# Kernel optimization log

Hardware: AMD Instinct MI355X
Metric: run time of the kernel (lower is better)

## Reference

```python
import jax, jax.numpy as jnp
import numpy as np

B, S, H, E = 2, 4096, 2048, 8


def setup_inputs() -> dict:
    key = jax.random.key(0)
    k1, k2, k3 = jax.random.split(key, 3)
    x = jax.random.normal(k1, (B, S, H), dtype=jnp.float32)
    w_router = jax.random.normal(k2, (E, H), dtype=jnp.float32) * (1.0 / np.sqrt(H))
    # nn.Linear weight layout: [out_features, in_features] per expert -> [E, H, H]
    w_experts = jax.random.normal(k3, (E, H, H), dtype=jnp.float32) * (1.0 / np.sqrt(H))
    return {"x": x, "w_router": w_router, "w_experts": w_experts}


def reference(x, w_router, w_experts):
    # router logits: x @ W_r^T  -> [B, S, E]
    logits = jnp.einsum('bsh,eh->bse', x, w_router)
    idx = jnp.argmax(logits, axis=-1)  # [B, S] top-1 expert per token
    # dense all-expert outputs (matches original which evaluates every expert):
    # expert_e(x) = x @ W_e^T -> [B, S, E, H]
    all_out = jnp.einsum('bsh,efh->bsef', x, w_experts)
    # masked sum over one-hot mask == gather of the selected expert output
    out = jnp.take_along_axis(all_out, idx[:, :, None, None], axis=2)[:, :, 0, :]
    return out
```

## Files before the change

### kernel.cpp

```cpp
#include <hip/hip_runtime.h>
#include <hip/hip_bf16.h>
#include <cstdint>

#define T_TOK 8192
#define H_DIM 2048
#define N_EXP 8
#define FLAGBIT 0x80000000u

typedef __attribute__((ext_vector_type(4))) float f32x4;
typedef __attribute__((ext_vector_type(8))) short bf16x8;

__device__ __forceinline__ unsigned short f2bf(float f) {
  unsigned int u = __builtin_bit_cast(unsigned int, f);
  u += 0x7fffu + ((u >> 16) & 1u);
  return (unsigned short)(u >> 16);
}

__device__ __forceinline__ unsigned cvtpk(float lo, float hi) {
  unsigned r;
  asm("v_cvt_pk_bf16_f32 %0, %1, %2" : "=v"(r) : "v"(lo), "v"(hi));
  return r;
}

#define GLL(SRC, DST) __builtin_amdgcn_global_load_lds( \
    (const __attribute__((address_space(1))) void*)(SRC), \
    (__attribute__((address_space(3))) void*)(DST), 16, 0, 0)

__global__ __launch_bounds__(256) void k_pre(const float* __restrict__ x,
    const float* __restrict__ wr, const float* __restrict__ we,
    unsigned short* __restrict__ xb, unsigned short* __restrict__ wb,
    int* __restrict__ idx)
{
  __shared__ char smem[65536];
  const int bid = blockIdx.x;
  if (bid >= 512) {
    auto* LDS3 = (__attribute__((address_space(3))) char*)smem;
    const char* LP = (const char*)smem;
    const int wv = threadIdx.x >> 6, l = threadIdx.x & 63;
    const size_t base = (size_t)(bid - 512) * 131072;
    const char* src = (const char*)we + base + wv * 8192 + l * 16;
    unsigned short* dstp = wb + (base >> 2) + wv * 2048 + l * 4;
#pragma unroll
    for (int i = 0; i < 8; ++i)
      GLL(src + i * 1024, LDS3 + wv * 8192 + i * 1024);
    for (int c = 0; c < 4; ++c) {
      const int b = (c & 1) * 32768;
      if (c < 3) {
        const char* s2 = src + (c + 1) * 32768;
        auto* d2 = LDS3 + (b ^ 32768) + wv * 8192;
#pragma unroll
        for (int i = 0; i < 8; ++i) GLL(s2 + i * 1024, d2 + i * 1024);
        asm volatile("s_waitcnt vmcnt(8)" ::: "memory");
      } else {
        asm volatile("s_waitcnt vmcnt(0)" ::: "memory");
      }
#pragma unroll
      for (int i = 0; i < 8; ++i) {
        const f32x4 v = *reinterpret_cast<const f32x4*>(LP + b + wv * 8192 + i * 1024 + l * 16);
        uint2 r;
        r.x = cvtpk(v[0], v[1]);
        r.y = cvtpk(v[2], v[3]);
        *reinterpret_cast<uint2*>(dstp + c * 8192 + i * 256) = r;
      }
    }
    return;
  }
  float* swr = (float*)smem;
#pragma unroll
  for (int i = 0; i < 16; ++i) {
    const int o = (threadIdx.x + i * 256) * 4;
    *reinterpret_cast<float4*>(&swr[o]) = *reinterpret_cast<const float4*>(&wr[o]);
  }
  __syncthreads();
  const int wv = threadIdx.x >> 6, lane = threadIdx.x & 63;
  const int t0 = (bid * 4 + wv) * 4;
  float acc[4][N_EXP];
#pragma unroll
  for (int tt = 0; tt < 4; ++tt)
#pragma unroll
    for (int e = 0; e < N_EXP; ++e) acc[tt][e] = 0.f;
#pragma unroll
  for (int c = 0; c < H_DIM / 256; ++c) {
    const int h = c * 256 + lane * 4;
    float4 wvv[N_EXP];
#pragma unroll
    for (int e = 0; e < N_EXP; ++e)
      wvv[e] = *reinterpret_cast<const float4*>(&swr[e * H_DIM + h]);
#pragma unroll
    for (int tt = 0; tt < 4; ++tt) {
      const float4 xv = *reinterpret_cast<const float4*>(x + (size_t)(t0 + tt) * H_DIM + h);
      ushort4 bv;
      bv.x = f2bf(xv.x); bv.y = f2bf(xv.y); bv.z = f2bf(xv.z); bv.w = f2bf(xv.w);
      *reinterpret_cast<ushort4*>(xb + (size_t)(t0 + tt) * H_DIM + h) = bv;
#pragma unroll
      for (int e = 0; e < N_EXP; ++e) {
        acc[tt][e] = fmaf(xv.x, wvv[e].x, acc[tt][e]);
        acc[tt][e] = fmaf(xv.y, wvv[e].y, acc[tt][e]);
        acc[tt][e] = fmaf(xv.z, wvv[e].z, acc[tt][e]);
        acc[tt][e] = fmaf(xv.w, wvv[e].w, acc[tt][e]);
      }
    }
  }
#pragma unroll
  for (int off = 32; off >= 1; off >>= 1)
#pragma unroll
    for (int tt = 0; tt < 4; ++tt)
#pragma unroll
      for (int e = 0; e < N_EXP; ++e) acc[tt][e] += __shfl_xor(acc[tt][e], off, 64);
  if (lane == 0) {
#pragma unroll
    for (int tt = 0; tt < 4; ++tt) {
      float best = acc[tt][0]; int be = 0;
#pragma unroll
      for (int e = 1; e < N_EXP; ++e) if (acc[tt][e] > best) { best = acc[tt][e]; be = e; }
      idx[t0 + tt] = be;
    }
  }
}

__global__ __launch_bounds__(1024) void k_sort(const int* __restrict__ idx,
    int* __restrict__ tlist, int* __restrict__ estar, int* __restrict__ mlo,
    int* __restrict__ mhi, int* __restrict__ rpos, int* __restrict__ rtile,
    int* __restrict__ rtc)
{
  __shared__ int wc[N_EXP][128];
  __shared__ int wbase[N_EXP][128];
  __shared__ int sTot[N_EXP];
  __shared__ int off[N_EXP + 1];
  __shared__ int sE[32], sCnt[N_EXP], sBase[N_EXP];
  const int tid = threadIdx.x, w = tid >> 6, l = tid & 63;
  int myE[8];
#pragma unroll
  for (int j = 0; j < 8; ++j) {
    myE[j] = idx[j * 1024 + tid];
#pragma unroll
    for (int e = 0; e < N_EXP; ++e) {
      const unsigned long long bm = __ballot(myE[j] == e);
      if (l == e) wc[e][j * 16 + w] = __popcll(bm);
    }
  }
  __syncthreads();
  if (tid < N_EXP) {
    int s = 0;
    for (int k = 0; k < 128; ++k) { wbase[tid][k] = s; s += wc[tid][k]; }
    sTot[tid] = s;
  }
  __syncthreads();
  if (tid == 0) {
    off[0] = 0;
    for (int e = 0; e < N_EXP; ++e) off[e + 1] = off[e] + sTot[e];
  }
  __syncthreads();
#pragma unroll
  for (int j = 0; j < 8; ++j) {
    int rank = 0;
#pragma unroll
    for (int e = 0; e < N_EXP; ++e) {
      const unsigned long long bm = __ballot(myE[j] == e);
      if (myE[j] == e) rank = __popcll(bm & ((1ull << l) - 1ull));
    }
    tlist[off[myE[j]] + wbase[myE[j]][j * 16 + w] + rank] = j * 1024 + tid;
  }
  if (tid < 32) {
    const int lo = tid * 256, hi = lo + 256;
    int bl = -1, bE = 0, bLo = 0, bHi = 0;
#pragma unroll
    for (int e = 0; e < N_EXP; ++e) {
      const int a = off[e] > lo ? off[e] : lo;
      const int b = off[e + 1] < hi ? off[e + 1] : hi;
      if (b - a > bl) { bl = b - a; bE = e; bLo = a - lo; bHi = b - lo; }
    }
    sE[tid] = bE; estar[tid] = bE; mlo[tid] = bLo; mhi[tid] = bHi;
  }
  __syncthreads();
  if (tid < N_EXP) {
    int cnt = 0;
    for (int t = 0; t < 32; ++t) {
      if (sE[t] == tid) continue;
      const int lo = t * 256, hi = lo + 256;
      const int a = off[tid] > lo ? off[tid] : lo;
      const int b = off[tid + 1] < hi ? off[tid + 1] : hi;
      if (b > a) cnt += b - a;
    }
    sCnt[tid] = cnt;
  }
  __syncthreads();
  if (tid == 0) {
    int base = 0, ntile = 0;
    for (int e = 0; e < N_EXP; ++e) {
      sBase[e] = base;
      const int pt = (sCnt[e] + 127) >> 7;
      for (int k = 0; k < pt; ++k) rtile[ntile++] = e;
      base += pt << 7;
    }
    *rtc = ntile;
  }
  __syncthreads();
  if (tid < N_EXP && sCnt[tid] > 0) {
    int ptr = sBase[tid], firstp = -1;
    for (int t = 0; t < 32; ++t) {
      if (sE[t] == tid) continue;
      const int lo = t * 256, hi = lo + 256;
      const int a = off[tid] > lo ? off[tid] : lo;
      const int b = off[tid + 1] < hi ? off[tid + 1] : hi;
      for (int p = a; p < b; ++p) { if (firstp < 0) firstp = p; rpos[ptr++] = p; }
    }
    const int end = sBase[tid] + (((sCnt[tid] + 127) >> 7) << 7);
    for (; ptr < end; ++ptr) rpos[ptr] = (int)((unsigned)firstp | FLAGBIT);
  }
}

__global__ __launch_bounds__(256) void k_zero_min(const int* __restrict__ rpos,
    const int* __restrict__ tlist, const int* __restrict__ rtc,
    float* __restrict__ out)
{
  const int nslots = (*rtc) << 7;
  const float4 z = {0.f, 0.f, 0.f, 0.f};
  for (int s = blockIdx.x; s < nslots; s += 256) {
    const int ent = rpos[s];
    if ((unsigned)ent & FLAGBIT) continue;
    const int tok = tlist[ent];
    float* op = out + (size_t)tok * H_DIM;
    for (int i = threadIdx.x; i < H_DIM / 4; i += 256)
      reinterpret_cast<float4*>(op)[i] = z;
  }
}

__global__ __launch_bounds__(1024, 4) void k_gemm(const unsigned short* __restrict__ xb,
    const unsigned short* __restrict__ wb, const int* __restrict__ tlist,
    const int* __restrict__ estar, const int* __restrict__ mlo, const int* __restrict__ mhi,
    const int* __restrict__ rpos, const int* __restrict__ rtile, const int* __restrict__ rtc,
    float* __restrict__ out)
{
  __shared__ short lds[65536];
  const int bid = blockIdx.x;
  const int tid = threadIdx.x;
  const int l = tid & 63, wv = tid >> 6;
  const int l16 = l & 15, g16 = l >> 4;
  const char* LP = (const char*)lds;
  auto* LDS3 = (__attribute__((address_space(3))) char*)lds;

  if (bid < 256) {
    const int mt = (bid & 7) * 4 + ((bid >> 3) & 3);
    const int nt = bid >> 5;
    const int m0 = mt * 256, f0 = nt * 256;
    const int e = estar[mt], mLo = mlo[mt], mHi = mhi[mt];
    const int wm = wv >> 2, wn = wv & 3;

    const int ch = (g16 ^ ((l16 >> 1) & 3)) << 4;
    const int aRd = (wm * 64 + l16) * 64 + ch;
    const int bRd = 16384 + (wn * 64 + l16) * 64 + ch;

    const int csrc = (((l & 3) ^ ((l >> 3) & 3))) * 8;
    const int srow = l >> 2;
    const int tokA = tlist[m0 + wv * 16 + srow];
    const unsigned short* aS = xb + (size_t)tokA * H_DIM + csrc;
    const unsigned short* bS = wb + (size_t)e * H_DIM * H_DIM
                                  + (size_t)(f0 + wv * 16 + srow) * H_DIM + csrc;
    const int dA = wv * 1024;
    const int dB = 16384 + wv * 1024;

    f32x4 acc[4][4];
#pragma unroll
    for (int mf = 0; mf < 4; ++mf)
#pragma unroll
      for (int nf = 0; nf < 4; ++nf) acc[mf][nf] = (f32x4){0.f, 0.f, 0.f, 0.f};

    GLL(aS +  0, LDS3 + 0 * 32768 + dA);  GLL(bS +  0, LDS3 + 0 * 32768 + dB);
    GLL(aS + 32, LDS3 + 1 * 32768 + dA);  GLL(bS + 32, LDS3 + 1 * 32768 + dB);
    GLL(aS + 64, LDS3 + 2 * 32768 + dA);  GLL(bS + 64, LDS3 + 2 * 32768 + dB);
    asm volatile("s_waitcnt vmcnt(4)" ::: "memory");
    __builtin_amdgcn_sched_barrier(0);
    __builtin_amdgcn_s_barrier();
    __builtin_amdgcn_sched_barrier(0);

    for (int t = 0; t < 64; ++t) {
      const int buf  = (t & 3) * 32768;
      const int nbuf = ((t + 3) & 3) * 32768;
      const int kk   = ((t + 3) & 63) * 32;
      bf16x8 af[4], bf[4];
#pragma unroll
      for (int mf = 0; mf < 4; ++mf)
        af[mf] = *reinterpret_cast<const bf16x8*>(LP + buf + aRd + mf * 1024);
#pragma unroll
      for (int nf = 0; nf < 4; ++nf)
        bf[nf] = *reinterpret_cast<const bf16x8*>(LP + buf + bRd + nf * 1024);
      GLL(aS + kk, LDS3 + nbuf + dA);
      GLL(bS + kk, LDS3 + nbuf + dB);
      __builtin_amdgcn_s_setprio(1);
#pragma unroll
      for (int mf = 0; mf < 4; ++mf)
#pragma unroll
        for (int nf = 0; nf < 4; ++nf)
          acc[mf][nf] = __builtin_amdgcn_mfma_f32_16x16x32_bf16(af[mf], bf[nf], acc[mf][nf], 0, 0, 0);
      __builtin_amdgcn_s_setprio(0);
      asm volatile("s_waitcnt vmcnt(4)" ::: "memory");
      __builtin_amdgcn_sched_barrier(0);
      __builtin_amdgcn_s_barrier();
      __builtin_amdgcn_sched_barrier(0);
    }

#pragma unroll
    for (int mf = 0; mf < 4; ++mf) {
#pragma unroll
      for (int r = 0; r < 4; ++r) {
        const int row = wm * 64 + mf * 16 + g16 * 4 + r;
        if (row >= mLo && row < mHi) {
          const int t2 = tlist[m0 + row];
          float* op = out + (size_t)t2 * H_DIM + f0 + wn * 64 + l16;
#pragma unroll
          for (int nf = 0; nf < 4; ++nf) op[nf * 16] = acc[mf][nf][r];
        }
      }
    }
    return;
  }

  const int bid2 = bid - 256;
  const int bx = bid2 >> 4;
  if (bx >= *rtc) return;
  const int f0 = ((bid2 >> 1) & 7) * 256;
  const int kc = bid2 & 1;
  const int e = rtile[bx];
  const int wm = wv >> 2, wn = wv & 3;
  const int sw = l16 & 7;
  const int ch0 = ((0 + g16) ^ sw) << 4, ch1 = ((4 + g16) ^ sw) << 4;
  const int csrc8 = ((l & 7) ^ ((l >> 3) & 7)) * 8;
  const int srow8 = l >> 3;

  const unsigned short* aS;
  {
    const int ent = rpos[bx * 128 + wv * 8 + srow8];
    const int tok = tlist[ent & 0x7fffffff];
    aS = xb + (size_t)tok * H_DIM + csrc8;
  }
  const unsigned short* bS0 = wb + (size_t)e * H_DIM * H_DIM
                                 + (size_t)(f0 + wv * 8 + srow8) * H_DIM + csrc8;
  const unsigned short* bS1 = bS0 + (size_t)128 * H_DIM;

  f32x4 acc[2][4];
#pragma unroll
  for (int mf = 0; mf < 2; ++mf)
#pragma unroll
    for (int nf = 0; nf < 4; ++nf) acc[mf][nf] = (f32x4){0.f, 0.f, 0.f, 0.f};

  for (int it = 0; it < 16; ++it) {
    const int kk = kc * 1024 + it * 64;
    __syncthreads();
    GLL(aS + kk, LDS3 + wv * 1024);
    GLL(bS0 + kk, LDS3 + 16384 + wv * 1024);
    GLL(bS1 + kk, LDS3 + 16384 + 16384 + wv * 1024);
    __syncthreads();
    bf16x8 af[2][2];
#pragma unroll
    for (int mf = 0; mf < 2; ++mf) {
      af[mf][0] = *reinterpret_cast<const bf16x8*>(LP + (wm * 32 + mf * 16 + l16) * 128 + ch0);
      af[mf][1] = *reinterpret_cast<const bf16x8*>(LP + (wm * 32 + mf * 16 + l16) * 128 + ch1);
    }
#pragma unroll
    for (int nf = 0; nf < 4; ++nf) {
      const bf16x8 b0 = *reinterpret_cast<const bf16x8*>(LP + 16384 + (wn * 64 + nf * 16 + l16) * 128 + ch0);
      const bf16x8 b1 = *reinterpret_cast<const bf16x8*>(LP + 16384 + (wn * 64 + nf * 16 + l16) * 128 + ch1);
#pragma unroll
      for (int mf = 0; mf < 2; ++mf) {
        acc[mf][nf] = __builtin_amdgcn_mfma_f32_16x16x32_bf16(af[mf][0], b0, acc[mf][nf], 0, 0, 0);
        acc[mf][nf] = __builtin_amdgcn_mfma_f32_16x16x32_bf16(af[mf][1], b1, acc[mf][nf], 0, 0, 0);
      }
    }
  }
#pragma unroll
  for (int mf = 0; mf < 2; ++mf) {
#pragma unroll
    for (int r = 0; r < 4; ++r) {
      const int row = wm * 32 + mf * 16 + g16 * 4 + r;
      const int ent = rpos[bx * 128 + row];
      if (!((unsigned)ent & FLAGBIT)) {
        const int tok = tlist[ent];
        float* op = out + (size_t)tok * H_DIM + f0 + wn * 64 + l16;
#pragma unroll
        for (int nf = 0; nf < 4; ++nf) atomicAdd(op + nf * 16, acc[mf][nf][r]);
      }
    }
  }
}

extern "C" void kernel_launch(void* const* d_in, const int* in_sizes, int n_in,
                              void* d_out, int out_size, void* d_ws, size_t ws_size,
                              hipStream_t stream) {
  const float* x  = (const float*)d_in[0];
  const float* wr = (const float*)d_in[1];
  const float* we = (const float*)d_in[2];
  float* out = (float*)d_out;

  char* p = (char*)d_ws;
  unsigned short* xb = (unsigned short*)p; p += (size_t)T_TOK * H_DIM * 2;
  unsigned short* wb = (unsigned short*)p; p += (size_t)N_EXP * H_DIM * H_DIM * 2;
  int* idx    = (int*)p; p += T_TOK * 4;
  int* tlist  = (int*)p; p += T_TOK * 4;
  int* rpos   = (int*)p; p += T_TOK * 4;
  int* estar  = (int*)p; p += 32 * 4;
  int* mlo    = (int*)p; p += 32 * 4;
  int* mhi    = (int*)p; p += 32 * 4;
  int* rtile  = (int*)p; p += 64 * 4;
  int* rtc    = (int*)p; p += 64;

  k_pre<<<512 + 1024, 256, 0, stream>>>(x, wr, we, xb, wb, idx);
  k_sort<<<1, 1024, 0, stream>>>(idx, tlist, estar, mlo, mhi, rpos, rtile, rtc);
  k_zero_min<<<256, 256, 0, stream>>>(rpos, tlist, rtc, out);
  k_gemm<<<256 + 1024, 1024, 0, stream>>>(xb, wb, tlist, estar, mlo, mhi, rpos, rtile, rtc, out);
}
```

Baseline: 184.1 us.

## Shrink GEMM workgroups to 256 threads with 128x128 tiles and more blocks

The main grouped GEMM now uses 256-thread workgroups computing 128x128 output tiles instead of 1024-thread workgroups on 256x256 tiles. Each wave issues twice as many async global-to-LDS loads, and LDS use is halved. The remainder path for mixed-expert tiles is reworked the same way: 4 waves, K step 32 instead of 64, and a 4x8 fragment accumulator per wave. The aim is more concurrent blocks per CU and better latency hiding, at the cost of less data reuse per tile and more blocks to schedule.

```diff
diff --git a/kernel.cpp b/kernel.cpp
--- a/kernel.cpp
+++ b/kernel.cpp
@@ -226,39 +226,49 @@
   }
 }
 
-__global__ __launch_bounds__(1024, 4) void k_gemm(const unsigned short* __restrict__ xb,
+__global__ __launch_bounds__(256) void k_gemm(const unsigned short* __restrict__ xb,
     const unsigned short* __restrict__ wb, const int* __restrict__ tlist,
     const int* __restrict__ estar, const int* __restrict__ mlo, const int* __restrict__ mhi,
     const int* __restrict__ rpos, const int* __restrict__ rtile, const int* __restrict__ rtc,
     float* __restrict__ out)
 {
-  __shared__ short lds[65536];
+  __shared__ short lds[32768];
   const int bid = blockIdx.x;
   const int tid = threadIdx.x;
   const int l = tid & 63, wv = tid >> 6;
   const int l16 = l & 15, g16 = l >> 4;
   const char* LP = (const char*)lds;
   auto* LDS3 = (__attribute__((address_space(3))) char*)lds;
-
-  if (bid < 256) {
-    const int mt = (bid & 7) * 4 + ((bid >> 3) & 3);
-    const int nt = bid >> 5;
-    const int m0 = mt * 256, f0 = nt * 256;
-    const int e = estar[mt], mLo = mlo[mt], mHi = mhi[mt];
-    const int wm = wv >> 2, wn = wv & 3;
-
-    const int ch = (g16 ^ ((l16 >> 1) & 3)) << 4;
+  const int csrc = ((l & 3) ^ ((l >> 3) & 3)) * 8;
+  const int ch = (g16 ^ ((l16 >> 1) & 3)) << 4;
+
+  if (bid < 1024) {
+    const int idx8 = bid >> 3;
+    const int mt = (bid & 7) * 8 + (idx8 >> 4);
+    const int nt = idx8 & 15;
+    const int m0 = mt * 128, f0 = nt * 128;
+    const int par = mt >> 1, half = (mt & 1) * 128;
+    const int e = estar[par];
+    const int mLo = mlo[par] - half, mHi = mhi[par] - half;
+    const int wm = wv >> 1, wn = wv & 1;
+
     const int aRd = (wm * 64 + l16) * 64 + ch;
-    const int bRd = 16384 + (wn * 64 + l16) * 64 + ch;
-
-    const int csrc = (((l & 3) ^ ((l >> 3) & 3))) * 8;
+    const int bRd = 8192 + (wn * 64 + l16) * 64 + ch;
+
     const int srow = l >> 2;
-    const int tokA = tlist[m0 + wv * 16 + srow];
-    const unsigned short* aS = xb + (size_t)tokA * H_DIM + csrc;
-    const unsigned short* bS = wb + (size_t)e * H_DIM * H_DIM
-                                  + (size_t)(f0 + wv * 16 + srow) * H_DIM + csrc;
-    const int dA = wv * 1024;
-    const int dB = 16384 + wv * 1024;
+    const unsigned short* aS[2];
+#pragma unroll
+    for (int j = 0; j < 2; ++j) {
+      const int tok = tlist[m0 + wv * 32 + j * 16 + srow];
+      aS[j] = xb + (size_t)tok * H_DIM + csrc;
+    }
+    const unsigned short* bS[2];
+#pragma unroll
+    for (int j = 0; j < 2; ++j)
+      bS[j] = wb + (size_t)e * H_DIM * H_DIM
+                 + (size_t)(f0 + wv * 32 + j * 16 + srow) * H_DIM + csrc;
+    const int dA0 = wv * 2048, dA1 = wv * 2048 + 1024;
+    const int dB0 = 8192 + wv * 2048, dB1 = 8192 + wv * 2048 + 1024;
 
     f32x4 acc[4][4];
 #pragma unroll
@@ -266,17 +276,20 @@
 #pragma unroll
       for (int nf = 0; nf < 4; ++nf) acc[mf][nf] = (f32x4){0.f, 0.f, 0.f, 0.f};
 
-    GLL(aS +  0, LDS3 + 0 * 32768 + dA);  GLL(bS +  0, LDS3 + 0 * 32768 + dB);
-    GLL(aS + 32, LDS3 + 1 * 32768 + dA);  GLL(bS + 32, LDS3 + 1 * 32768 + dB);
-    GLL(aS + 64, LDS3 + 2 * 32768 + dA);  GLL(bS + 64, LDS3 + 2 * 32768 + dB);
-    asm volatile("s_waitcnt vmcnt(4)" ::: "memory");
+#pragma unroll
+    for (int t0i = 0; t0i < 3; ++t0i) {
+      const int bb = t0i * 16384, kk = t0i * 32;
+      GLL(aS[0] + kk, LDS3 + bb + dA0);  GLL(aS[1] + kk, LDS3 + bb + dA1);
+      GLL(bS[0] + kk, LDS3 + bb + dB0);  GLL(bS[1] + kk, LDS3 + bb + dB1);
+    }
+    asm volatile("s_waitcnt vmcnt(8)" ::: "memory");
     __builtin_amdgcn_sched_barrier(0);
     __builtin_amdgcn_s_barrier();
     __builtin_amdgcn_sched_barrier(0);
 
     for (int t = 0; t < 64; ++t) {
-      const int buf  = (t & 3) * 32768;
-      const int nbuf = ((t + 3) & 3) * 32768;
+      const int buf  = (t & 3) * 16384;
+      const int nbuf = ((t + 3) & 3) * 16384;
       const int kk   = ((t + 3) & 63) * 32;
       bf16x8 af[4], bf[4];
 #pragma unroll
@@ -285,8 +298,8 @@
 #pragma unroll
       for (int nf = 0; nf < 4; ++nf)
         bf[nf] = *reinterpret_cast<const bf16x8*>(LP + buf + bRd + nf * 1024);
-      GLL(aS + kk, LDS3 + nbuf + dA);
-      GLL(bS + kk, LDS3 + nbuf + dB);
+      GLL(aS[0] + kk, LDS3 + nbuf + dA0);  GLL(aS[1] + kk, LDS3 + nbuf + dA1);
+      GLL(bS[0] + kk, LDS3 + nbuf + dB0);  GLL(bS[1] + kk, LDS3 + nbuf + dB1);
       __builtin_amdgcn_s_setprio(1);
 #pragma unroll
       for (int mf = 0; mf < 4; ++mf)
@@ -294,7 +307,7 @@
         for (int nf = 0; nf < 4; ++nf)
           acc[mf][nf] = __builtin_amdgcn_mfma_f32_16x16x32_bf16(af[mf], bf[nf], acc[mf][nf], 0, 0, 0);
       __builtin_amdgcn_s_setprio(0);
-      asm volatile("s_waitcnt vmcnt(4)" ::: "memory");
+      asm volatile("s_waitcnt vmcnt(8)" ::: "memory");
       __builtin_amdgcn_sched_barrier(0);
       __builtin_amdgcn_s_barrier();
       __builtin_amdgcn_sched_barrier(0);
@@ -316,69 +329,66 @@
     return;
   }
 
-  const int bid2 = bid - 256;
+  const int bid2 = bid - 1024;
   const int bx = bid2 >> 4;
   if (bx >= *rtc) return;
   const int f0 = ((bid2 >> 1) & 7) * 256;
   const int kc = bid2 & 1;
   const int e = rtile[bx];
-  const int wm = wv >> 2, wn = wv & 3;
-  const int sw = l16 & 7;
-  const int ch0 = ((0 + g16) ^ sw) << 4, ch1 = ((4 + g16) ^ sw) << 4;
-  const int csrc8 = ((l & 7) ^ ((l >> 3) & 7)) * 8;
-  const int srow8 = l >> 3;
-
-  const unsigned short* aS;
-  {
-    const int ent = rpos[bx * 128 + wv * 8 + srow8];
+  const int wm = wv >> 1, wn = wv & 1;
+  const int srow = l >> 2;
+
+  const unsigned short* aS[2];
+#pragma unroll
+  for (int j = 0; j < 2; ++j) {
+    const int ent = rpos[bx * 128 + wv * 32 + j * 16 + srow];
     const int tok = tlist[ent & 0x7fffffff];
-    aS = xb + (size_t)tok * H_DIM + csrc8;
-  }
-  const unsigned short* bS0 = wb + (size_t)e * H_DIM * H_DIM
-                                 + (size_t)(f0 + wv * 8 + srow8) * H_DIM + csrc8;
-  const unsigned short* bS1 = bS0 + (size_t)128 * H_DIM;
-
-  f32x4 acc[2][4];
-#pragma unroll
-  for (int mf = 0; mf < 2; ++mf)
-#pragma unroll
-    for (int nf = 0; nf < 4; ++nf) acc[mf][nf] = (f32x4){0.f, 0.f, 0.f, 0.f};
-
-  for (int it = 0; it < 16; ++it) {
-    const int kk = kc * 1024 + it * 64;
+    aS[j] = xb + (size_t)tok * H_DIM + csrc;
+  }
+  const unsigned short* bS[4];
+#pragma unroll
+  for (int j = 0; j < 4; ++j)
+    bS[j] = wb + (size_t)e * H_DIM * H_DIM
+               + (size_t)(f0 + wv * 64 + j * 16 + srow) * H_DIM + csrc;
+
+  f32x4 acc[4][8];
+#pragma unroll
+  for (int mf = 0; mf < 4; ++mf)
+#pragma unroll
+    for (int nf = 0; nf < 8; ++nf) acc[mf][nf] = (f32x4){0.f, 0.f, 0.f, 0.f};
+
+  for (int it = 0; it < 32; ++it) {
+    const int kk = kc * 1024 + it * 32;
     __syncthreads();
-    GLL(aS + kk, LDS3 + wv * 1024);
-    GLL(bS0 + kk, LDS3 + 16384 + wv * 1024);
-    GLL(bS1 + kk, LDS3 + 16384 + 16384 + wv * 1024);
+#pragma unroll
+    for (int j = 0; j < 2; ++j) GLL(aS[j] + kk, LDS3 + wv * 2048 + j * 1024);
+#pragma unroll
+    for (int j = 0; j < 4; ++j) GLL(bS[j] + kk, LDS3 + 8192 + wv * 4096 + j * 1024);
     __syncthreads();
-    bf16x8 af[2][2];
-#pragma unroll
-    for (int mf = 0; mf < 2; ++mf) {
-      af[mf][0] = *reinterpret_cast<const bf16x8*>(LP + (wm * 32 + mf * 16 + l16) * 128 + ch0);
-      af[mf][1] = *reinterpret_cast<const bf16x8*>(LP + (wm * 32 + mf * 16 + l16) * 128 + ch1);
-    }
-#pragma unroll
-    for (int nf = 0; nf < 4; ++nf) {
-      const bf16x8 b0 = *reinterpret_cast<const bf16x8*>(LP + 16384 + (wn * 64 + nf * 16 + l16) * 128 + ch0);
-      const bf16x8 b1 = *reinterpret_cast<const bf16x8*>(LP + 16384 + (wn * 64 + nf * 16 + l16) * 128 + ch1);
-#pragma unroll
-      for (int mf = 0; mf < 2; ++mf) {
-        acc[mf][nf] = __builtin_amdgcn_mfma_f32_16x16x32_bf16(af[mf][0], b0, acc[mf][nf], 0, 0, 0);
-        acc[mf][nf] = __builtin_amdgcn_mfma_f32_16x16x32_bf16(af[mf][1], b1, acc[mf][nf], 0, 0, 0);
-      }
-    }
-  }
-#pragma unroll
-  for (int mf = 0; mf < 2; ++mf) {
+    bf16x8 af[4];
+#pragma unroll
+    for (int mf = 0; mf < 4; ++mf)
+      af[mf] = *reinterpret_cast<const bf16x8*>(LP + (wm * 64 + mf * 16 + l16) * 64 + ch);
+#pragma unroll
+    for (int nf = 0; nf < 8; ++nf) {
+      const bf16x8 b0 = *reinterpret_cast<const bf16x8*>(
+          LP + 8192 + (wn * 128 + nf * 16 + l16) * 64 + ch);
+#pragma unroll
+      for (int mf = 0; mf < 4; ++mf)
+        acc[mf][nf] = __builtin_amdgcn_mfma_f32_16x16x32_bf16(af[mf], b0, acc[mf][nf], 0, 0, 0);
+    }
+  }
+#pragma unroll
+  for (int mf = 0; mf < 4; ++mf) {
 #pragma unroll
     for (int r = 0; r < 4; ++r) {
-      const int row = wm * 32 + mf * 16 + g16 * 4 + r;
+      const int row = wm * 64 + mf * 16 + g16 * 4 + r;
       const int ent = rpos[bx * 128 + row];
       if (!((unsigned)ent & FLAGBIT)) {
         const int tok = tlist[ent];
-        float* op = out + (size_t)tok * H_DIM + f0 + wn * 64 + l16;
-#pragma unroll
-        for (int nf = 0; nf < 4; ++nf) atomicAdd(op + nf * 16, acc[mf][nf][r]);
+        float* op = out + (size_t)tok * H_DIM + f0 + wn * 128 + l16;
+#pragma unroll
+        for (int nf = 0; nf < 8; ++nf) atomicAdd(op + nf * 16, acc[mf][nf][r]);
       }
     }
   }
@@ -407,5 +417,5 @@
   k_pre<<<512 + 1024, 256, 0, stream>>>(x, wr, we, xb, wb, idx);
   k_sort<<<1, 1024, 0, stream>>>(idx, tlist, estar, mlo, mhi, rpos, rtile, rtc);
   k_zero_min<<<256, 256, 0, stream>>>(rpos, tlist, rtc, out);
-  k_gemm<<<256 + 1024, 1024, 0, stream>>>(xb, wb, tlist, estar, mlo, mhi, rpos, rtile, rtc, out);
-}
+  k_gemm<<<1024 + 1024, 256, 0, stream>>>(xb, wb, tlist, estar, mlo, mhi, rpos, rtile, rtc, out);
+}
```

Result: slower. 243.6 us (+32.3%).
